# Kernel tuning notes

Hardware: AMD Instinct MI355X
Metric: run time of the kernel (lower is better)

Reference implementation:

```python
import jax, jax.numpy as jnp
import numpy as np

B_SZ, D, U, NBR, MH, RH = 16384, 256, 32, 8, 512, 256  # batch, latent, u_dim, branches, meas hidden, rnn hidden
NY = 8 * 2 + 4  # num_prod*2 + num_inj
LN_EPS = 1e-5


def setup_inputs() -> dict:
    key = jax.random.key(0)
    ks = jax.random.split(key, 16)
    inp = {
        "zt": jax.random.normal(ks[0], (B_SZ, D), jnp.float32),
        "dt": jax.random.uniform(ks[1], (1, 1), jnp.float32, 0.1, 1.0),
        "ut": jax.random.normal(ks[2], (B_SZ, U), jnp.float32),
        # stacked per-branch parameters
        "gates": jax.random.normal(ks[3], (NBR, D), jnp.float32) * 0.1,
        "W1": jax.random.normal(ks[4], (NBR, MH, D), jnp.float32) / np.sqrt(D),
        "b1": jnp.zeros((NBR, MH), jnp.float32),
        "ln_g": jnp.ones((NBR, MH), jnp.float32),
        "ln_b": jnp.zeros((NBR, MH), jnp.float32),
        "W2": jax.random.normal(ks[5], (NBR, RH, MH), jnp.float32) / np.sqrt(MH),
        "b2": jnp.zeros((NBR, RH), jnp.float32),
        "lam_r": jnp.zeros((NBR, RH), jnp.float32),
        "lam_i": jax.random.normal(ks[6], (NBR, RH), jnp.float32) * 0.1,
        "rnn_B": jax.random.normal(ks[7], (NBR, RH, RH + U), jnp.float32) / np.sqrt(RH + U),
        "W_out": jax.random.normal(ks[8], (NBR, D, RH), jnp.float32) / np.sqrt(RH),
        "C": jax.random.normal(ks[9], (NY, D), jnp.float32) / np.sqrt(D),
        "Dm": jax.random.normal(ks[10], (NY, U), jnp.float32) / np.sqrt(U),
    }
    return inp


def reference(zt, dt, ut, gates, W1, b1, ln_g, ln_b, W2, b2, lam_r, lam_i, rnn_B, W_out, C, Dm):
    ut_dt = ut * dt                                           # [B, U]
    # spectral gating, all branches at once: [NBR, B, D]
    zg = zt[None, :, :] * jax.nn.sigmoid(gates)[:, None, :]
    # measurement MLP: Linear -> LayerNorm -> GELU (exact) -> Linear
    x = jnp.einsum('nbd,nhd->nbh', zg, W1) + b1[:, None, :]   # [NBR, B, MH]
    mu = jnp.mean(x, axis=-1, keepdims=True)
    var = jnp.mean((x - mu) ** 2, axis=-1, keepdims=True)
    x = (x - mu) / jnp.sqrt(var + LN_EPS) * ln_g[:, None, :] + ln_b[:, None, :]
    x = jax.nn.gelu(x, approximate=False)
    g = jnp.einsum('nbh,nrh->nbr', x, W2) + b2[:, None, :]    # [NBR, B, RH]
    # concat control and apply input matrix B_n
    ut_b = jnp.broadcast_to(ut_dt[None], (gates.shape[0],) + ut_dt.shape)
    inp = jnp.concatenate([g, ut_b], axis=-1)                 # [NBR, B, RH+U]
    b_inp = jnp.einsum('nbi,nri->nbr', inp, rnn_B)            # [NBR, B, RH]
    # single diagonal complex RNN step from h0 = 0:
    #   h_real = 0*lam.r - 0*lam.i + b_inp = b_inp ; h_imag = 0  (lambda drops out)
    h_real = b_inp
    zt1 = jnp.einsum('nbr,ndr->bd', h_real, W_out)            # sum over branches
    yt1 = zt1 @ C.T + ut_dt @ Dm.T
    return zt1, yt1
```

## Files before the change

### kernel.cpp

```cpp
#include <hip/hip_runtime.h>
#include <math.h>

#define B_TOT 16384
#define DD    256
#define UU    32
#define NBR   8
#define MH    512
#define RH    256
#define KIN   288
#define NY    20

typedef unsigned short u16;
typedef __attribute__((ext_vector_type(8))) short bfx8;
typedef __attribute__((ext_vector_type(4))) short bfx4;
typedef __attribute__((ext_vector_type(4))) float fx4;

#define MFMA(a, b, c) __builtin_amdgcn_mfma_f32_16x16x32_bf16((a), (b), (c), 0, 0, 0)

__device__ __forceinline__ u16 f2bf(float f) {
  __bf16 h = (__bf16)f;
  return __builtin_bit_cast(u16, h);
}
__device__ __forceinline__ float fsigmoid(float x) {
  return __builtin_amdgcn_rcpf(1.f + __expf(-x));
}
__device__ __forceinline__ float fgelu(float v) {
  float t = v * v;
  float z = v * __builtin_fmaf(t, 0.07135481627f, 1.5957691216f);
  float p = __expf(z);
  return v - v * __builtin_amdgcn_rcpf(p + 1.f);
}
__device__ __forceinline__ void gload16(const void* g, void* l) {
  __builtin_amdgcn_global_load_lds((const __attribute__((address_space(1))) unsigned int*)(g),
                                   (__attribute__((address_space(3))) unsigned int*)(l),
                                   16, 0, 0);
}

__global__ __launch_bounds__(256)
void skolr_prep(const float* __restrict__ W1, const float* __restrict__ W2,
                const float* __restrict__ rnnB, const float* __restrict__ Wout,
                const float* __restrict__ gates, const float* __restrict__ zt,
                u16* __restrict__ w1g, u16* __restrict__ w2b, u16* __restrict__ bb,
                u16* __restrict__ wotb, u16* __restrict__ ztb)
{
  long i = (long)(blockIdx.x * 256 + threadIdx.x) * 8;
  const long E0 = 1048576;
  const long E1 = 2097152;
  const long E2 = 2686976;
  const long E3 = 3211264;
  const long E4 = 7405568;
  if (i >= E4) return;
  if (i < E0) {
    int n = (int)(i >> 17), h = (int)((i >> 8) & 511), d = (int)(i & 255);
    const float* gp = gates + n * DD + d;
    float4 g0 = *(const float4*)gp, g1 = *(const float4*)(gp + 4);
    float4 a = *(const float4*)(W1 + i), b = *(const float4*)(W1 + i + 4);
    bfx8 v;
    v[0] = f2bf(a.x * fsigmoid(g0.x)); v[1] = f2bf(a.y * fsigmoid(g0.y));
    v[2] = f2bf(a.z * fsigmoid(g0.z)); v[3] = f2bf(a.w * fsigmoid(g0.w));
    v[4] = f2bf(b.x * fsigmoid(g1.x)); v[5] = f2bf(b.y * fsigmoid(g1.y));
    v[6] = f2bf(b.z * fsigmoid(g1.z)); v[7] = f2bf(b.w * fsigmoid(g1.w));
    u16* dst = w1g + (size_t)n * 131072
             + ((((h >> 4) << 3) + (d >> 5)) << 9) + ((h & 15) << 3) + (((d >> 3) & 3) << 7);
    *(bfx8*)dst = v;
    return;
  }
  const float* src; u16* dst; long off;
  if (i < E1) {
    off = i - E0;
    int n = (int)(off >> 17), r = (int)((off >> 9) & 255), k = (int)(off & 511);
    src = W2 + off;
    dst = w2b + (size_t)n * 131072
        + ((((r >> 4) << 4) + (k >> 5)) << 9) + ((r & 15) << 3) + (((k >> 3) & 3) << 7);
  } else if (i < E2) {
    off = i - E1;
    int o = (int)off;
    int n = o / 73728, rem = o - n * 73728;
    int r = rem / KIN, k = rem - r * KIN;
    src = rnnB + off;
    dst = bb + (size_t)n * 73728
        + (((r >> 4) * 9 + (k >> 5)) << 9) + ((r & 15) << 3) + (((k >> 3) & 3) << 7);
  } else if (i < E3) {
    off = i - E2;
    int n = (int)(off >> 16), rem = (int)(off & 65535);
    int d = rem >> 8, r = rem & 255;
    src = Wout + off;
    dst = wotb + ((((d >> 4) << 6) + (n << 3) + (r >> 5)) << 9)
        + ((d & 15) << 3) + (((r >> 3) & 3) << 7);
  } else {
    off = i - E3;
    src = zt + off;
    dst = ztb + off;
  }
  float4 a = *(const float4*)src, b = *(const float4*)(src + 4);
  bfx8 v;
  v[0] = f2bf(a.x); v[1] = f2bf(a.y); v[2] = f2bf(a.z); v[3] = f2bf(a.w);
  v[4] = f2bf(b.x); v[5] = f2bf(b.y); v[6] = f2bf(b.z); v[7] = f2bf(b.w);
  *(bfx8*)dst = v;
}

__global__ __launch_bounds__(512, 2)
void skolr_fused(const u16* __restrict__ ztb, const float* __restrict__ dtp,
                 const float* __restrict__ ut,
                 const u16* __restrict__ w1g, const float* __restrict__ b1,
                 const float* __restrict__ lng, const float* __restrict__ lnb,
                 const u16* __restrict__ w2g, const float* __restrict__ b2v,
                 const u16* __restrict__ rnnb, u16* __restrict__ bing)
{
  __shared__ __align__(16) char smX[65536];
  __shared__ __align__(16) float smR[1024];
  const int tid = threadIdx.x;
  const int w  = tid >> 6;
  const int l  = tid & 63;
  const int lr = l & 15;
  const int lg = l >> 4;
  const int n  = blockIdx.x;
  const int b0 = blockIdx.y * 64;

  #pragma unroll
  for (int j = 0; j < 4; ++j) {
    int q = (w << 2) + j;
    int r = (q << 1) + (l >> 5);
    const u16* src = ztb + (size_t)(b0 + r) * DD + (((l & 31) ^ (r & 7)) << 3);
    gload16(src, smX + (q << 10));
  }
  __syncthreads();

  fx4 acc1[4][4];
  #pragma unroll
  for (int mt = 0; mt < 4; ++mt)
    #pragma unroll
    for (int nt = 0; nt < 4; ++nt)
      acc1[mt][nt] = (fx4){0.f, 0.f, 0.f, 0.f};
  {
    const u16* w1pk = w1g + (size_t)n * 131072;
    #pragma unroll
    for (int kk = 0; kk < 8; ++kk) {
      bfx8 bfr[4];
      #pragma unroll
      for (int nt = 0; nt < 4; ++nt) {
        int b = nt * 16 + lr;
        bfr[nt] = *(const bfx8*)(smX + b * 512 + ((((kk << 2) + lg) ^ (b & 7)) << 4));
      }
      #pragma unroll
      for (int mt = 0; mt < 4; ++mt) {
        int mtile = (mt < 2 ? (w << 1) + mt : 16 + (w << 1) + (mt - 2));
        bfx8 af = *(const bfx8*)(w1pk + (((mtile << 3) + kk) << 9) + (l << 3));
        #pragma unroll
        for (int nt = 0; nt < 4; ++nt)
          acc1[mt][nt] = MFMA(af, bfr[nt], acc1[mt][nt]);
      }
    }
  }
  #pragma unroll
  for (int mt = 0; mt < 4; ++mt) {
    int hb = (mt < 2 ? (w << 5) + mt * 16 : 256 + (w << 5) + (mt - 2) * 16) + (lg << 2);
    fx4 bv = *(const fx4*)(b1 + n * MH + hb);
    #pragma unroll
    for (int nt = 0; nt < 4; ++nt)
      acc1[mt][nt] += bv;
  }

  #pragma unroll
  for (int nt = 0; nt < 4; ++nt) {
    float s1 = 0.f, s2 = 0.f;
    #pragma unroll
    for (int mt = 0; mt < 4; ++mt)
      #pragma unroll
      for (int r = 0; r < 4; ++r) { float v = acc1[mt][nt][r]; s1 += v; s2 += v * v; }
    s1 += __shfl_xor(s1, 16); s1 += __shfl_xor(s1, 32);
    s2 += __shfl_xor(s2, 16); s2 += __shfl_xor(s2, 32);
    if (l < 16) { smR[w * 64 + nt * 16 + l] = s1; smR[512 + w * 64 + nt * 16 + l] = s2; }
  }
  __syncthreads();

  float meanv[4], rstdv[4];
  #pragma unroll
  for (int nt = 0; nt < 4; ++nt) {
    float ms = 0.f, ss = 0.f;
    #pragma unroll
    for (int wv = 0; wv < 8; ++wv) {
      ms += smR[wv * 64 + nt * 16 + lr];
      ss += smR[512 + wv * 64 + nt * 16 + lr];
    }
    float mean = ms * (1.f / 512.f);
    meanv[nt] = mean;
    rstdv[nt] = rsqrtf(ss * (1.f / 512.f) - mean * mean + 1e-5f);
  }
  #pragma unroll
  for (int mt = 0; mt < 4; ++mt) {
    int htile = (mt < 2 ? (w << 5) + mt * 16 : 256 + (w << 5) + (mt - 2) * 16);
    int hb = htile + (lg << 2);
    fx4 g4 = *(const fx4*)(lng + n * MH + hb);
    fx4 e4 = *(const fx4*)(lnb + n * MH + hb);
    #pragma unroll
    for (int nt = 0; nt < 4; ++nt) {
      #pragma unroll
      for (int r = 0; r < 4; ++r) {
        float v = (acc1[mt][nt][r] - meanv[nt]) * rstdv[nt] * g4[r] + e4[r];
        acc1[mt][nt][r] = fgelu(v);
      }
      int b = nt * 16 + lr;
      bfx4 p;
      p[0] = f2bf(acc1[mt][nt][0]); p[1] = f2bf(acc1[mt][nt][1]);
      p[2] = f2bf(acc1[mt][nt][2]); p[3] = f2bf(acc1[mt][nt][3]);
      int chunk6 = (htile >> 3) + (lg >> 1);
      *(bfx4*)(smX + b * 1024 + ((chunk6 ^ (b & 7)) << 4) + ((lg & 1) << 3)) = p;
    }
  }
  __syncthreads();

  const int r0 = w << 5;
  fx4 acc2[2][4];
  #pragma unroll
  for (int mt = 0; mt < 2; ++mt)
    #pragma unroll
    for (int nt = 0; nt < 4; ++nt)
      acc2[mt][nt] = (fx4){0.f, 0.f, 0.f, 0.f};
  {
    const u16* w2pk = w2g + (size_t)n * 131072;
    #pragma unroll
    for (int kk = 0; kk < 16; ++kk) {
      bfx8 xb[4];
      #pragma unroll
      for (int nt = 0; nt < 4; ++nt) {
        int b = nt * 16 + lr;
        xb[nt] = *(const bfx8*)(smX + b * 1024 + ((((kk << 2) + lg) ^ (b & 7)) << 4));
      }
      #pragma unroll
      for (int mt = 0; mt < 2; ++mt) {
        bfx8 af = *(const bfx8*)(w2pk + (((((w << 1) + mt) << 4) + kk) << 9) + (l << 3));
        #pragma unroll
        for (int nt = 0; nt < 4; ++nt)
          acc2[mt][nt] = MFMA(af, xb[nt], acc2[mt][nt]);
      }
    }
  }
  #pragma unroll
  for (int mt = 0; mt < 2; ++mt) {
    fx4 bz = *(const fx4*)(b2v + n * RH + r0 + mt * 16 + (lg << 2));
    #pragma unroll
    for (int nt = 0; nt < 4; ++nt)
      acc2[mt][nt] += bz;
  }
  __syncthreads();

  #pragma unroll
  for (int mt = 0; mt < 2; ++mt)
    #pragma unroll
    for (int nt = 0; nt < 4; ++nt) {
      int b = nt * 16 + lr;
      bfx4 p;
      p[0] = f2bf(acc2[mt][nt][0]); p[1] = f2bf(acc2[mt][nt][1]);
      p[2] = f2bf(acc2[mt][nt][2]); p[3] = f2bf(acc2[mt][nt][3]);
      int chunk5 = ((r0 + mt * 16) >> 3) + (lg >> 1);
      *(bfx4*)(smX + b * 512 + ((chunk5 ^ (b & 7)) << 4) + ((lg & 1) << 3)) = p;
    }
  __syncthreads();

  const float dtv = dtp[0];
  bfx8 ufrag[4];
  #pragma unroll
  for (int nt = 0; nt < 4; ++nt) {
    const float* up = ut + (size_t)(b0 + nt * 16 + lr) * UU + (lg << 3);
    float4 u0 = *(const float4*)up;
    float4 u1 = *(const float4*)(up + 4);
    bfx8 v;
    v[0] = f2bf(u0.x * dtv); v[1] = f2bf(u0.y * dtv);
    v[2] = f2bf(u0.z * dtv); v[3] = f2bf(u0.w * dtv);
    v[4] = f2bf(u1.x * dtv); v[5] = f2bf(u1.y * dtv);
    v[6] = f2bf(u1.z * dtv); v[7] = f2bf(u1.w * dtv);
    ufrag[nt] = v;
  }

  fx4 acc3[2][4];
  #pragma unroll
  for (int mt = 0; mt < 2; ++mt)
    #pragma unroll
    for (int nt = 0; nt < 4; ++nt)
      acc3[mt][nt] = (fx4){0.f, 0.f, 0.f, 0.f};
  {
    const u16* rpk = rnnb + (size_t)n * 73728;
    #pragma unroll
    for (int kk = 0; kk < 8; ++kk) {
      bfx8 gb[4];
      #pragma unroll
      for (int nt = 0; nt < 4; ++nt) {
        int b = nt * 16 + lr;
        gb[nt] = *(const bfx8*)(smX + b * 512 + ((((kk << 2) + lg) ^ (b & 7)) << 4));
      }
      #pragma unroll
      for (int mt = 0; mt < 2; ++mt) {
        bfx8 af = *(const bfx8*)(rpk + (((((w << 1) + mt) * 9) + kk) << 9) + (l << 3));
        #pragma unroll
        for (int nt = 0; nt < 4; ++nt)
          acc3[mt][nt] = MFMA(af, gb[nt], acc3[mt][nt]);
      }
    }
    #pragma unroll
    for (int mt = 0; mt < 2; ++mt) {
      bfx8 af = *(const bfx8*)(rpk + (((((w << 1) + mt) * 9) + 8) << 9) + (l << 3));
      #pragma unroll
      for (int nt = 0; nt < 4; ++nt)
        acc3[mt][nt] = MFMA(af, ufrag[nt], acc3[mt][nt]);
    }
  }
  #pragma unroll
  for (int mt = 0; mt < 2; ++mt)
    #pragma unroll
    for (int nt = 0; nt < 4; ++nt) {
      int b = nt * 16 + lr;
      bfx4 p;
      p[0] = f2bf(acc3[mt][nt][0]); p[1] = f2bf(acc3[mt][nt][1]);
      p[2] = f2bf(acc3[mt][nt][2]); p[3] = f2bf(acc3[mt][nt][3]);
      int chunk5 = ((r0 + mt * 16) >> 3) + (lg >> 1);
      *(bfx4*)(smX + 32768 + b * 512 + ((chunk5 ^ (b & 7)) << 4) + ((lg & 1) << 3)) = p;
    }
  __syncthreads();

  {
    int c = tid & 31;
    #pragma unroll
    for (int j = 0; j < 4; ++j) {
      int row = (tid >> 5) + j * 16;
      int4 v = *(const int4*)(smX + 32768 + row * 512 + (c << 4));
      *(int4*)(bing + (size_t)(b0 + row) * 2048 + n * 256 + c * 8) = v;
    }
  }
}

__global__ __launch_bounds__(512, 4)
void skolr_final(const u16* __restrict__ bing, const u16* __restrict__ wotb,
                 const float* __restrict__ ut, const float* __restrict__ dtp,
                 const float* __restrict__ Cm, const float* __restrict__ Dm,
                 float* __restrict__ outp)
{
  __shared__ __align__(16) char sB[32768];
  const int tid = threadIdx.x;
  const int w  = tid >> 6;
  const int l  = tid & 63;
  const int lr = l & 15;
  const int lg = l >> 4;
  const int b0 = blockIdx.x * 32;
  const int d0 = w << 5;

  fx4 acc[2][2];
  #pragma unroll
  for (int mt = 0; mt < 2; ++mt)
    #pragma unroll
    for (int nt = 0; nt < 2; ++nt)
      acc[mt][nt] = (fx4){0.f, 0.f, 0.f, 0.f};

  const int srow = tid >> 5;
  const int scol = tid & 31;
  #define STAGE(buf, ks)                                                        \
    {                                                                           \
      _Pragma("unroll")                                                         \
      for (int j = 0; j < 2; ++j) {                                             \
        const u16* src = bing + (size_t)(b0 + srow + j * 16) * 2048             \
                              + ((ks) << 8) + (scol << 3);                      \
        void* ldst = sB + (buf) * 16384 + (w << 10) + (j << 13);                \
        gload16(src, ldst);                                                     \
      }                                                                         \
    }

  STAGE(0, 0)
  for (int ks = 0; ks < 8; ++ks) {
    if (ks < 7) {
      STAGE((ks + 1) & 1, ks + 1)
      asm volatile("s_waitcnt vmcnt(2)" ::: "memory");
    } else {
      asm volatile("s_waitcnt vmcnt(0)" ::: "memory");
    }
    __builtin_amdgcn_s_barrier();
    const char* cur = sB + (ks & 1) * 16384;
    #pragma unroll
    for (int kk = 0; kk < 8; ++kk) {
      bfx8 bf[2];
      #pragma unroll
      for (int nt = 0; nt < 2; ++nt) {
        int b = nt * 16 + lr;
        bf[nt] = *(const bfx8*)(cur + b * 512 + ((((kk << 2) + lg) ^ (b & 7)) << 4));
      }
      #pragma unroll
      for (int mt = 0; mt < 2; ++mt) {
        bfx8 af = *(const bfx8*)(wotb + (((((w << 1) + mt) << 6) + (ks << 3) + kk) << 9) + (l << 3));
        #pragma unroll
        for (int nt = 0; nt < 2; ++nt)
          acc[mt][nt] = MFMA(af, bf[nt], acc[mt][nt]);
      }
    }
    __builtin_amdgcn_s_barrier();
  }

  #pragma unroll
  for (int mt = 0; mt < 2; ++mt)
    #pragma unroll
    for (int nt = 0; nt < 2; ++nt) {
      int bl = nt * 16 + lr;
      int d  = d0 + mt * 16 + (lg << 2);
      *(fx4*)(outp + (size_t)(b0 + bl) * DD + d) = acc[mt][nt];
      bfx4 p;
      p[0] = f2bf(acc[mt][nt][0]); p[1] = f2bf(acc[mt][nt][1]);
      p[2] = f2bf(acc[mt][nt][2]); p[3] = f2bf(acc[mt][nt][3]);
      int chunk5 = d >> 3;
      *(bfx4*)(sB + bl * 512 + ((chunk5 ^ (bl & 7)) << 4) + ((lg & 1) << 3)) = p;
    }
  __syncthreads();

  const float dtv = dtp[0];
  for (int i = tid; i < 32 * NY; i += 512) {
    int b = i / NY;
    int y = i - b * NY;
    float s = 0.f;
    #pragma unroll 4
    for (int dc = 0; dc < 32; ++dc) {
      bfx8 zv = *(const bfx8*)(sB + b * 512 + ((dc ^ (b & 7)) << 4));
      const float* cp = Cm + y * DD + dc * 8;
      float4 c0 = *(const float4*)cp;
      float4 c1 = *(const float4*)(cp + 4);
      float z0 = (float)__builtin_bit_cast(__bf16, (u16)zv[0]);
      float z1 = (float)__builtin_bit_cast(__bf16, (u16)zv[1]);
      float z2 = (float)__builtin_bit_cast(__bf16, (u16)zv[2]);
      float z3 = (float)__builtin_bit_cast(__bf16, (u16)zv[3]);
      float z4 = (float)__builtin_bit_cast(__bf16, (u16)zv[4]);
      float z5 = (float)__builtin_bit_cast(__bf16, (u16)zv[5]);
      float z6 = (float)__builtin_bit_cast(__bf16, (u16)zv[6]);
      float z7 = (float)__builtin_bit_cast(__bf16, (u16)zv[7]);
      s += z0 * c0.x + z1 * c0.y + z2 * c0.z + z3 * c0.w;
      s += z4 * c1.x + z5 * c1.y + z6 * c1.z + z7 * c1.w;
    }
    const float* up = ut + (size_t)(b0 + b) * UU;
    const float* dp = Dm + y * UU;
    float s2 = 0.f;
    #pragma unroll
    for (int u = 0; u < UU; u += 4) {
      float4 uu = *(const float4*)(up + u);
      float4 dd = *(const float4*)(dp + u);
      s2 += uu.x * dd.x + uu.y * dd.y + uu.z * dd.z + uu.w * dd.w;
    }
    outp[(size_t)B_TOT * DD + (size_t)(b0 + b) * NY + y] = s + dtv * s2;
  }
}

extern "C" void kernel_launch(void* const* d_in, const int* in_sizes, int n_in,
                              void* d_out, int out_size, void* d_ws, size_t ws_size,
                              hipStream_t stream)
{
  (void)in_sizes; (void)n_in; (void)out_size; (void)ws_size;
  const float* zt    = (const float*)d_in[0];
  const float* dtp   = (const float*)d_in[1];
  const float* ut    = (const float*)d_in[2];
  const float* gates = (const float*)d_in[3];
  const float* W1    = (const float*)d_in[4];
  const float* b1    = (const float*)d_in[5];
  const float* lng   = (const float*)d_in[6];
  const float* lnb   = (const float*)d_in[7];
  const float* W2    = (const float*)d_in[8];
  const float* b2    = (const float*)d_in[9];
  const float* rnnB  = (const float*)d_in[12];
  const float* Wout  = (const float*)d_in[13];
  const float* Cm    = (const float*)d_in[14];
  const float* Dm    = (const float*)d_in[15];
  float* outp = (float*)d_out;
  char* ws = (char*)d_ws;

  u16* w1g  = (u16*)(ws + 0);
  u16* w2b  = (u16*)(ws + 2097152);
  u16* bb   = (u16*)(ws + 4194304);
  u16* wotb = (u16*)(ws + 5373952);
  u16* ztb  = (u16*)(ws + 6422528);
  u16* bing = (u16*)(ws + 14811136);

  skolr_prep<<<3616, 256, 0, stream>>>(W1, W2, rnnB, Wout, gates, zt,
                                       w1g, w2b, bb, wotb, ztb);
  skolr_fused<<<dim3(8, 256), 512, 0, stream>>>(ztb, dtp, ut, w1g, b1, lng, lnb,
                                                w2b, b2, bb, bing);
  skolr_final<<<512, 512, 0, stream>>>(bing, wotb, ut, dtp, Cm, Dm, outp);
}
```

Measured before the change: 310.7 us.

## Halve fused-kernel LDS by splitting second GEMM and store bing directly

The fused kernel's shared buffer shrinks from 64KB to 32KB. The GELU output is staged in two halves, and the second GEMM runs as two K-halves separated by a barrier. Launch bounds are raised from 2 to 6 blocks, `s_setprio` is raised around the MFMA loops, and the RNN-input result goes straight from registers to global memory in the same swizzled layout instead of through LDS. The aim is higher occupancy and less LDS traffic, at the cost of extra barriers, uncoalesced 8-byte global stores, and a tighter register budget that could cause spills given the 64-float accumulator tile.

```diff
diff --git a/kernel.cpp b/kernel.cpp
--- a/kernel.cpp
+++ b/kernel.cpp
@@ -99,7 +99,7 @@
   *(bfx8*)dst = v;
 }
 
-__global__ __launch_bounds__(512, 2)
+__global__ __launch_bounds__(512, 6)
 void skolr_fused(const u16* __restrict__ ztb, const float* __restrict__ dtp,
                  const float* __restrict__ ut,
                  const u16* __restrict__ w1g, const float* __restrict__ b1,
@@ -107,7 +107,7 @@
                  const u16* __restrict__ w2g, const float* __restrict__ b2v,
                  const u16* __restrict__ rnnb, u16* __restrict__ bing)
 {
-  __shared__ __align__(16) char smX[65536];
+  __shared__ __align__(16) char smX[32768];
   __shared__ __align__(16) float smR[1024];
   const int tid = threadIdx.x;
   const int w  = tid >> 6;
@@ -134,6 +134,7 @@
       acc1[mt][nt] = (fx4){0.f, 0.f, 0.f, 0.f};
   {
     const u16* w1pk = w1g + (size_t)n * 131072;
+    __builtin_amdgcn_s_setprio(1);
     #pragma unroll
     for (int kk = 0; kk < 8; ++kk) {
       bfx8 bfr[4];
@@ -151,6 +152,7 @@
           acc1[mt][nt] = MFMA(af, bfr[nt], acc1[mt][nt]);
       }
     }
+    __builtin_amdgcn_s_setprio(0);
   }
   #pragma unroll
   for (int mt = 0; mt < 4; ++mt) {
@@ -189,25 +191,29 @@
   }
   #pragma unroll
   for (int mt = 0; mt < 4; ++mt) {
-    int htile = (mt < 2 ? (w << 5) + mt * 16 : 256 + (w << 5) + (mt - 2) * 16);
-    int hb = htile + (lg << 2);
+    int hb = (mt < 2 ? (w << 5) + mt * 16 : 256 + (w << 5) + (mt - 2) * 16) + (lg << 2);
     fx4 g4 = *(const fx4*)(lng + n * MH + hb);
     fx4 e4 = *(const fx4*)(lnb + n * MH + hb);
     #pragma unroll
-    for (int nt = 0; nt < 4; ++nt) {
+    for (int nt = 0; nt < 4; ++nt)
       #pragma unroll
       for (int r = 0; r < 4; ++r) {
         float v = (acc1[mt][nt][r] - meanv[nt]) * rstdv[nt] * g4[r] + e4[r];
         acc1[mt][nt][r] = fgelu(v);
       }
+  }
+
+  #pragma unroll
+  for (int mt = 0; mt < 2; ++mt)
+    #pragma unroll
+    for (int nt = 0; nt < 4; ++nt) {
       int b = nt * 16 + lr;
       bfx4 p;
       p[0] = f2bf(acc1[mt][nt][0]); p[1] = f2bf(acc1[mt][nt][1]);
       p[2] = f2bf(acc1[mt][nt][2]); p[3] = f2bf(acc1[mt][nt][3]);
-      int chunk6 = (htile >> 3) + (lg >> 1);
-      *(bfx4*)(smX + b * 1024 + ((chunk6 ^ (b & 7)) << 4) + ((lg & 1) << 3)) = p;
-    }
-  }
+      int ch = (((w << 5) + mt * 16) >> 3) + (lg >> 1);
+      *(bfx4*)(smX + b * 512 + ((ch ^ (b & 7)) << 4) + ((lg & 1) << 3)) = p;
+    }
   __syncthreads();
 
   const int r0 = w << 5;
@@ -217,15 +223,16 @@
     #pragma unroll
     for (int nt = 0; nt < 4; ++nt)
       acc2[mt][nt] = (fx4){0.f, 0.f, 0.f, 0.f};
+  const u16* w2pk = w2g + (size_t)n * 131072;
   {
-    const u16* w2pk = w2g + (size_t)n * 131072;
-    #pragma unroll
-    for (int kk = 0; kk < 16; ++kk) {
+    __builtin_amdgcn_s_setprio(1);
+    #pragma unroll
+    for (int kk = 0; kk < 8; ++kk) {
       bfx8 xb[4];
       #pragma unroll
       for (int nt = 0; nt < 4; ++nt) {
         int b = nt * 16 + lr;
-        xb[nt] = *(const bfx8*)(smX + b * 1024 + ((((kk << 2) + lg) ^ (b & 7)) << 4));
+        xb[nt] = *(const bfx8*)(smX + b * 512 + ((((kk << 2) + lg) ^ (b & 7)) << 4));
       }
       #pragma unroll
       for (int mt = 0; mt < 2; ++mt) {
@@ -235,28 +242,50 @@
           acc2[mt][nt] = MFMA(af, xb[nt], acc2[mt][nt]);
       }
     }
-  }
-  #pragma unroll
-  for (int mt = 0; mt < 2; ++mt) {
-    fx4 bz = *(const fx4*)(b2v + n * RH + r0 + mt * 16 + (lg << 2));
-    #pragma unroll
-    for (int nt = 0; nt < 4; ++nt)
-      acc2[mt][nt] += bz;
-  }
-  __syncthreads();
-
-  #pragma unroll
-  for (int mt = 0; mt < 2; ++mt)
+    __builtin_amdgcn_s_setprio(0);
+  }
+  __syncthreads();
+
+  #pragma unroll
+  for (int mt = 2; mt < 4; ++mt)
     #pragma unroll
     for (int nt = 0; nt < 4; ++nt) {
       int b = nt * 16 + lr;
       bfx4 p;
-      p[0] = f2bf(acc2[mt][nt][0]); p[1] = f2bf(acc2[mt][nt][1]);
-      p[2] = f2bf(acc2[mt][nt][2]); p[3] = f2bf(acc2[mt][nt][3]);
-      int chunk5 = ((r0 + mt * 16) >> 3) + (lg >> 1);
-      *(bfx4*)(smX + b * 512 + ((chunk5 ^ (b & 7)) << 4) + ((lg & 1) << 3)) = p;
-    }
-  __syncthreads();
+      p[0] = f2bf(acc1[mt][nt][0]); p[1] = f2bf(acc1[mt][nt][1]);
+      p[2] = f2bf(acc1[mt][nt][2]); p[3] = f2bf(acc1[mt][nt][3]);
+      int ch = (((w << 5) + (mt - 2) * 16) >> 3) + (lg >> 1);
+      *(bfx4*)(smX + b * 512 + ((ch ^ (b & 7)) << 4) + ((lg & 1) << 3)) = p;
+    }
+  __syncthreads();
+
+  {
+    __builtin_amdgcn_s_setprio(1);
+    #pragma unroll
+    for (int kk = 8; kk < 16; ++kk) {
+      bfx8 xb[4];
+      #pragma unroll
+      for (int nt = 0; nt < 4; ++nt) {
+        int b = nt * 16 + lr;
+        xb[nt] = *(const bfx8*)(smX + b * 512 + (((((kk - 8) << 2) + lg) ^ (b & 7)) << 4));
+      }
+      #pragma unroll
+      for (int mt = 0; mt < 2; ++mt) {
+        bfx8 af = *(const bfx8*)(w2pk + (((((w << 1) + mt) << 4) + kk) << 9) + (l << 3));
+        #pragma unroll
+        for (int nt = 0; nt < 4; ++nt)
+          acc2[mt][nt] = MFMA(af, xb[nt], acc2[mt][nt]);
+      }
+    }
+    __builtin_amdgcn_s_setprio(0);
+  }
+  #pragma unroll
+  for (int mt = 0; mt < 2; ++mt) {
+    fx4 bz = *(const fx4*)(b2v + n * RH + r0 + mt * 16 + (lg << 2));
+    #pragma unroll
+    for (int nt = 0; nt < 4; ++nt)
+      acc2[mt][nt] += bz;
+  }
 
   const float dtv = dtp[0];
   bfx8 ufrag[4];
@@ -272,6 +301,20 @@
     v[6] = f2bf(u1.z * dtv); v[7] = f2bf(u1.w * dtv);
     ufrag[nt] = v;
   }
+  __syncthreads();
+
+  #pragma unroll
+  for (int mt = 0; mt < 2; ++mt)
+    #pragma unroll
+    for (int nt = 0; nt < 4; ++nt) {
+      int b = nt * 16 + lr;
+      bfx4 p;
+      p[0] = f2bf(acc2[mt][nt][0]); p[1] = f2bf(acc2[mt][nt][1]);
+      p[2] = f2bf(acc2[mt][nt][2]); p[3] = f2bf(acc2[mt][nt][3]);
+      int ch = ((r0 + mt * 16) >> 3) + (lg >> 1);
+      *(bfx4*)(smX + b * 512 + ((ch ^ (b & 7)) << 4) + ((lg & 1) << 3)) = p;
+    }
+  __syncthreads();
 
   fx4 acc3[2][4];
   #pragma unroll
@@ -281,6 +324,7 @@
       acc3[mt][nt] = (fx4){0.f, 0.f, 0.f, 0.f};
   {
     const u16* rpk = rnnb + (size_t)n * 73728;
+    __builtin_amdgcn_s_setprio(1);
     #pragma unroll
     for (int kk = 0; kk < 8; ++kk) {
       bfx8 gb[4];
@@ -304,29 +348,21 @@
       for (int nt = 0; nt < 4; ++nt)
         acc3[mt][nt] = MFMA(af, ufrag[nt], acc3[mt][nt]);
     }
-  }
+    __builtin_amdgcn_s_setprio(0);
+  }
+
   #pragma unroll
   for (int mt = 0; mt < 2; ++mt)
     #pragma unroll
     for (int nt = 0; nt < 4; ++nt) {
-      int b = nt * 16 + lr;
+      int bl = nt * 16 + lr;
       bfx4 p;
       p[0] = f2bf(acc3[mt][nt][0]); p[1] = f2bf(acc3[mt][nt][1]);
       p[2] = f2bf(acc3[mt][nt][2]); p[3] = f2bf(acc3[mt][nt][3]);
-      int chunk5 = ((r0 + mt * 16) >> 3) + (lg >> 1);
-      *(bfx4*)(smX + 32768 + b * 512 + ((chunk5 ^ (b & 7)) << 4) + ((lg & 1) << 3)) = p;
-    }
-  __syncthreads();
-
-  {
-    int c = tid & 31;
-    #pragma unroll
-    for (int j = 0; j < 4; ++j) {
-      int row = (tid >> 5) + j * 16;
-      int4 v = *(const int4*)(smX + 32768 + row * 512 + (c << 4));
-      *(int4*)(bing + (size_t)(b0 + row) * 2048 + n * 256 + c * 8) = v;
-    }
-  }
+      int ch  = ((r0 + mt * 16) >> 3) + (lg >> 1);
+      int pch = ch ^ (bl & 7);
+      *(bfx4*)(bing + (size_t)(b0 + bl) * 2048 + n * 256 + (pch << 3) + ((lg & 1) << 2)) = p;
+    }
 }
 
 __global__ __launch_bounds__(512, 4)
```

After: 678.9 us. 118% more time.
